# Kernel tuning notes

Hardware: AMD Instinct MI355X
Metric: run time of the kernel (lower is better)

Reference implementation:

```python
import jax, jax.numpy as jnp
import numpy as np

EPS = 1e-6
HEADS = 8


def _block_weights(gh, gw):
    # block centers at (i+0.5, j+0.5); 'cos' transform, column-normalized (sum over dim 0)
    ii, jj = np.meshgrid(np.arange(gh) + 0.5, np.arange(gw) + 0.5, indexing='ij')
    centers = np.stack([ii.ravel(), jj.ravel()], axis=-1)  # [N, 2]
    d = np.linalg.norm(centers[:, None, :] - centers[None, :, :], axis=-1)  # [N, N]
    mat = np.cos(d / d.max() * np.pi / 4.0)
    mat = mat / mat.sum(axis=0, keepdims=True)
    return jnp.asarray(mat, dtype=jnp.float32)


def setup_inputs() -> dict:
    key = jax.random.key(0)
    ks = jax.random.split(key, 5)
    B, N, W, C = 8, 256, 49, 512
    s = 1.0 / np.sqrt(C)
    return {
        'x': jax.random.normal(ks[0], (B, N, W, C), jnp.float32),
        'ln_g': jnp.ones((C,), jnp.float32),
        'ln_b': jnp.zeros((C,), jnp.float32),
        'w_qkv': jax.random.normal(ks[1], (3 * C, C), jnp.float32) * s,  # Linear(dim, 3*dim, bias=False)
        'lepe_w': jax.random.normal(ks[2], (C, 1, 5, 5), jnp.float32) * 0.2,  # depthwise 5x5
        'lepe_b': jnp.zeros((C,), jnp.float32),
        'w_out': jax.random.normal(ks[3], (C, C), jnp.float32) * s,
        'b_out': jnp.zeros((C,), jnp.float32),
    }


def reference(x, ln_g, ln_b, w_qkv, lepe_w, lepe_b, w_out, b_out):
    B, N, Wn, C = x.shape
    H = HEADS
    D = C // H
    gh = gw = int(round(N ** 0.5))   # grid of window blocks
    wh = ww = int(round(Wn ** 0.5))  # tokens per window side

    # LayerNorm over channel dim (torch eps=1e-5, biased var)
    mu = x.mean(-1, keepdims=True)
    var = x.var(-1, keepdims=True)
    xn = (x - mu) / jnp.sqrt(var + 1e-5) * ln_g + ln_b

    # qkv projection
    qkv = jnp.einsum('bnwc,oc->bnwo', xn, w_qkv)
    q, k, v = jnp.split(qkv, 3, axis=-1)  # each [B, N, W, C]

    # LePE: fold v to image [B, C, gh*wh, gw*ww], depthwise conv 5x5 pad 2, unfold back
    img = v.reshape(B, gh, gw, wh, ww, C).transpose(0, 5, 1, 3, 2, 4).reshape(B, C, gh * wh, gw * ww)
    lepe = jax.lax.conv_general_dilated(
        img, lepe_w, window_strides=(1, 1), padding=((2, 2), (2, 2)),
        dimension_numbers=('NCHW', 'OIHW', 'NCHW'), feature_group_count=C)
    lepe = lepe + lepe_b[None, :, None, None]
    lepe = lepe.reshape(B, C, gh, wh, gw, ww).transpose(0, 2, 4, 3, 5, 1).reshape(B, N, Wn, C)

    # ReLU + eps feature maps (qk_norm=False -> identity norms)
    q = jax.nn.relu(q) + EPS
    k = jax.nn.relu(k) + EPS

    # split heads: [B, H, N, W, D]
    def split_heads(t):
        return t.reshape(B, N, Wn, H, D).transpose(0, 3, 1, 2, 4)
    q, k, v = split_heads(q), split_heads(k), split_heads(v)

    # per-block k^T v state: [B, H, N, D, D]
    kv = jnp.einsum('bhnwd,bhnwe->bhnde', k, v)
    weight = _block_weights(gh, gw)  # [N, N]
    kv = jnp.einsum('ij,bhjde->bhide', weight, kv)

    k_sum = k.sum(axis=-2)  # [B, H, N, D]
    qk_sum = jnp.einsum('bhnwd,bhnd->bhnw', q, k_sum)[..., None]  # [B, H, N, W, 1]
    normalizer = jnp.einsum('ij,bhjwo->bhiwo', weight, qk_sum) + EPS

    out = jnp.einsum('bhnwd,bhnde->bhnwe', q, kv) / normalizer  # [B, H, N, W, D]
    out = out.transpose(0, 2, 3, 1, 4).reshape(B, N, Wn, C)
    out = out + lepe
    return jnp.einsum('bnwc,oc->bnwo', out, w_out) + b_out
```

## Files before the change

kernel.cpp:

```cpp
#include <hip/hip_runtime.h>
#include <cstdint>

typedef unsigned short u16;
typedef unsigned int   u32;
typedef u16   u16x8 __attribute__((ext_vector_type(8)));
typedef float f32x4 __attribute__((ext_vector_type(4)));
typedef __bf16 bf16x8 __attribute__((ext_vector_type(8)));

#define NB    256
#define WTOK  49
#define CH    512
#define HEADS 8
#define DH    64
#define TOK   100352
#define CO    1536

__device__ __forceinline__ u16 f2bf(float f) {
  u32 u = __float_as_uint(f);
  u = (u + 0x7FFFu + ((u >> 16) & 1u)) >> 16;
  return (u16)u;
}
__device__ __forceinline__ float bf2f(u16 u) { return __uint_as_float(((u32)u) << 16); }

__device__ __forceinline__ void load_lds16(const void* g, void* l) {
  __builtin_amdgcn_global_load_lds(
      reinterpret_cast<__attribute__((address_space(1))) void*>(reinterpret_cast<uintptr_t>(g)),
      reinterpret_cast<__attribute__((address_space(3))) void*>(reinterpret_cast<uintptr_t>(l)),
      16, 0, 0);
}

__global__ void cvt_f32_bf16(const float* __restrict__ in, u16* __restrict__ out, int n8) {
  int i = blockIdx.x * 256 + threadIdx.x;
  if (i < n8) {
    f32x4 a = *(const f32x4*)(in + (long)i * 8);
    f32x4 b = *(const f32x4*)(in + (long)i * 8 + 4);
    u16x8 o;
    o[0]=f2bf(a[0]); o[1]=f2bf(a[1]); o[2]=f2bf(a[2]); o[3]=f2bf(a[3]);
    o[4]=f2bf(b[0]); o[5]=f2bf(b[1]); o[6]=f2bf(b[2]); o[7]=f2bf(b[3]);
    *(u16x8*)(out + (long)i * 8) = o;
  }
}

__global__ void prep_wle(const float* __restrict__ lepe_w, float* __restrict__ wle) {
  int i = blockIdx.x * 256 + threadIdx.x;
  if (i < 12800) {
    int c = i / 25, kk = i % 25;
    wle[kk * 512 + c] = lepe_w[i];
  }
}

__global__ void weight_kernel(u16* __restrict__ Wbf, float* __restrict__ Wt) {
  int j = blockIdx.x, i = threadIdx.x;
  float iy = (float)(i >> 4) + 0.5f, ix = (float)(i & 15) + 0.5f;
  float jy = (float)(j >> 4) + 0.5f, jx = (float)(j & 15) + 0.5f;
  float dy = iy - jy, dx = ix - jx;
  float d = sqrtf(dy * dy + dx * dx);
  const float dmax = 21.213203435596427f;
  float m = cosf(d * (0.78539816339744831f / dmax));
  __shared__ float red[256];
  red[i] = m;
  __syncthreads();
  for (int s = 128; s > 0; s >>= 1) {
    if (i < s) red[i] += red[i + s];
    __syncthreads();
  }
  float w = m / red[0];
  Wbf[i * 256 + j] = f2bf(w);
  Wt[j * 256 + i] = w;
}

__global__ __launch_bounds__(256) void ln_kernel(const float* __restrict__ x,
                                                 const float* __restrict__ g,
                                                 const float* __restrict__ bta,
                                                 u16* __restrict__ xn) {
  int wave = threadIdx.x >> 6, lane = threadIdx.x & 63;
  long t = (long)blockIdx.x * 4 + wave;
  const float* xp = x + t * CH + lane * 8;
  f32x4 a = *(const f32x4*)xp;
  f32x4 b = *(const f32x4*)(xp + 4);
  float s  = a[0]+a[1]+a[2]+a[3]+b[0]+b[1]+b[2]+b[3];
  float sq = a[0]*a[0]+a[1]*a[1]+a[2]*a[2]+a[3]*a[3]+b[0]*b[0]+b[1]*b[1]+b[2]*b[2]+b[3]*b[3];
  for (int m = 1; m < 64; m <<= 1) { s += __shfl_xor(s, m); sq += __shfl_xor(sq, m); }
  float mu = s * (1.0f / 512.0f);
  float var = sq * (1.0f / 512.0f) - mu * mu;
  float rstd = rsqrtf(var + 1e-5f);
  const float* gp = g + lane * 8;
  const float* bp = bta + lane * 8;
  f32x4 g0 = *(const f32x4*)gp, g1 = *(const f32x4*)(gp + 4);
  f32x4 b0 = *(const f32x4*)bp, b1 = *(const f32x4*)(bp + 4);
  u16x8 o;
  o[0] = f2bf((a[0]-mu)*rstd*g0[0] + b0[0]);
  o[1] = f2bf((a[1]-mu)*rstd*g0[1] + b0[1]);
  o[2] = f2bf((a[2]-mu)*rstd*g0[2] + b0[2]);
  o[3] = f2bf((a[3]-mu)*rstd*g0[3] + b0[3]);
  o[4] = f2bf((b[0]-mu)*rstd*g1[0] + b1[0]);
  o[5] = f2bf((b[1]-mu)*rstd*g1[1] + b1[1]);
  o[6] = f2bf((b[2]-mu)*rstd*g1[2] + b1[2]);
  o[7] = f2bf((b[3]-mu)*rstd*g1[3] + b1[3]);
  *(u16x8*)(xn + t * CH + lane * 8) = o;
}

template <int KT>
__device__ __forceinline__ void kstep8(char* sm, const u16* sA, const u16* sB,
                                       int t, int lane_off, int wm, int wn,
                                       f32x4 (&acc)[8][4]) {
  const char* base = sm + (KT & 3) * 32768 + lane_off;
  char* wbp = sm + ((KT + 3) & 3) * 32768 + t * 16;
  if constexpr (KT + 3 < 16) {
    load_lds16(sA + (KT + 3) * 32, wbp);
    load_lds16(sA + (KT + 3) * 32 + 65536, wbp + 8192);
  }
  bf16x8 bfr[4], afr[4];
#pragma unroll
  for (int n = 0; n < 4; n++) bfr[n] = *(const bf16x8*)(base + 16384 + wn * 4096 + n * 1024);
#pragma unroll
  for (int m = 0; m < 4; m++) afr[m] = *(const bf16x8*)(base + wm * 8192 + m * 1024);
  __builtin_amdgcn_s_barrier();
  __builtin_amdgcn_s_setprio(1);
#pragma unroll
  for (int m = 0; m < 4; m++)
#pragma unroll
    for (int n = 0; n < 4; n++)
      acc[m][n] = __builtin_amdgcn_mfma_f32_16x16x32_bf16(afr[m], bfr[n], acc[m][n], 0, 0, 0);
  __builtin_amdgcn_s_setprio(0);
  __builtin_amdgcn_s_barrier();
  if constexpr (KT + 3 < 16) {
    load_lds16(sB + (KT + 3) * 32, wbp + 16384);
    load_lds16(sB + (KT + 3) * 32 + 65536, wbp + 24576);
  }
#pragma unroll
  for (int m = 0; m < 4; m++) afr[m] = *(const bf16x8*)(base + wm * 8192 + (4 + m) * 1024);
  __builtin_amdgcn_s_barrier();
  __builtin_amdgcn_s_setprio(1);
#pragma unroll
  for (int m = 0; m < 4; m++)
#pragma unroll
    for (int n = 0; n < 4; n++)
      acc[4 + m][n] = __builtin_amdgcn_mfma_f32_16x16x32_bf16(afr[m], bfr[n], acc[4 + m][n], 0, 0, 0);
  __builtin_amdgcn_s_setprio(0);
  if constexpr (KT < 13) {
    asm volatile("s_waitcnt vmcnt(8)" ::: "memory");
  } else if constexpr (KT == 13) {
    asm volatile("s_waitcnt vmcnt(4)" ::: "memory");
  } else if constexpr (KT == 14) {
    asm volatile("s_waitcnt vmcnt(0)" ::: "memory");
  }
  if constexpr (KT < 15) __builtin_amdgcn_s_barrier();
}

template <int EPI>
__global__ __launch_bounds__(512, 2)
void gemm8(const u16* __restrict__ A, const u16* __restrict__ B,
           void* __restrict__ C, const float* __restrict__ bias, int N, int nbn) {
  __shared__ __align__(16) char sm[131072];
  const int nwg = gridDim.x;
  const int bid = blockIdx.x;
  const int cpx = nwg >> 3;
  const int vid = (bid & 7) * cpx + (bid >> 3);
  const int bn = vid % nbn, bm = vid / nbn;
  const int t = threadIdx.x;
  const int lane = t & 63, wave = t >> 6;
  const int wm = wave >> 2, wn = wave & 3;
  const int fr = lane & 15, fq = lane >> 4;
  const int lane_off = (fr >> 1) * 128 + ((((fr & 1) << 2) + fq) ^ (fr >> 1)) * 16;
  const int sl = (t & 7) ^ ((t >> 3) & 7);
  const u16* sA = A + ((long)bm * 256 + ((t >> 3) << 1) + (sl >> 2)) * 512 + (sl & 3) * 8;
  const u16* sB = B + ((long)bn * 256 + ((t >> 3) << 1) + (sl >> 2)) * 512 + (sl & 3) * 8;
  f32x4 acc[8][4] = {};
#pragma unroll
  for (int kt = 0; kt < 3; kt++) {
    char* d = sm + kt * 32768 + t * 16;
    load_lds16(sA + kt * 32, d);
    load_lds16(sA + kt * 32 + 65536, d + 8192);
    load_lds16(sB + kt * 32, d + 16384);
    load_lds16(sB + kt * 32 + 65536, d + 24576);
  }
  asm volatile("s_waitcnt vmcnt(8)" ::: "memory");
  __builtin_amdgcn_s_barrier();
  kstep8<0>(sm, sA, sB, t, lane_off, wm, wn, acc);
  kstep8<1>(sm, sA, sB, t, lane_off, wm, wn, acc);
  kstep8<2>(sm, sA, sB, t, lane_off, wm, wn, acc);
  kstep8<3>(sm, sA, sB, t, lane_off, wm, wn, acc);
  kstep8<4>(sm, sA, sB, t, lane_off, wm, wn, acc);
  kstep8<5>(sm, sA, sB, t, lane_off, wm, wn, acc);
  kstep8<6>(sm, sA, sB, t, lane_off, wm, wn, acc);
  kstep8<7>(sm, sA, sB, t, lane_off, wm, wn, acc);
  kstep8<8>(sm, sA, sB, t, lane_off, wm, wn, acc);
  kstep8<9>(sm, sA, sB, t, lane_off, wm, wn, acc);
  kstep8<10>(sm, sA, sB, t, lane_off, wm, wn, acc);
  kstep8<11>(sm, sA, sB, t, lane_off, wm, wn, acc);
  kstep8<12>(sm, sA, sB, t, lane_off, wm, wn, acc);
  kstep8<13>(sm, sA, sB, t, lane_off, wm, wn, acc);
  kstep8<14>(sm, sA, sB, t, lane_off, wm, wn, acc);
  kstep8<15>(sm, sA, sB, t, lane_off, wm, wn, acc);
  const long r0 = (long)bm * 256 + wm * 128 + fq * 4;
  const int c0 = bn * 256 + wn * 64 + fr;
#pragma unroll
  for (int m = 0; m < 8; m++) {
#pragma unroll
    for (int n = 0; n < 4; n++) {
      int c = c0 + n * 16;
#pragma unroll
      for (int jj = 0; jj < 4; jj++) {
        long r = r0 + m * 16 + jj;
        float v = acc[m][n][jj];
        if (EPI == 1) {
          if (c < 1024) v = fmaxf(v, 0.0f) + 1e-6f;
          ((u16*)C)[r * N + c] = f2bf(v);
        } else if (EPI == 2) {
          ((float*)C)[r * N + c] = v + bias[c];
        } else {
          ((u16*)C)[r * N + c] = f2bf(v);
        }
      }
    }
  }
}

template <int EPI>
__global__ __launch_bounds__(256)
void gemm_bt(const u16* __restrict__ A, const u16* __restrict__ B,
             void* __restrict__ C, const float* __restrict__ bias,
             int M, int N, int K, long sAb, long sBb, long sCb) {
  __shared__ u16 As[128 * 32];
  __shared__ u16 Bs[128 * 32];
  const int tid = threadIdx.x;
  const int lane = tid & 63;
  const int wave = tid >> 6;
  const int fr = lane & 15, fq = lane >> 4;
  const int wr = (wave >> 1) * 64, wc = (wave & 1) * 64;
  const long bm = blockIdx.y, bn = blockIdx.x, bz = blockIdx.z;
  const u16* Ab = A + bz * sAb + bm * 128 * (long)K;
  const u16* Bb = B + bz * sBb + bn * 128 * (long)K;
  const int srow = tid >> 2;
  const int scol = (tid & 3) * 8;
  f32x4 acc[4][4] = {};
  for (int k0 = 0; k0 < K; k0 += 32) {
    load_lds16(Ab + (long)srow * K + k0 + scol, As + tid * 8);
    load_lds16(Ab + (long)(srow + 64) * K + k0 + scol, As + 2048 + tid * 8);
    load_lds16(Bb + (long)srow * K + k0 + scol, Bs + tid * 8);
    load_lds16(Bb + (long)(srow + 64) * K + k0 + scol, Bs + 2048 + tid * 8);
    __syncthreads();
    bf16x8 af[4], bf[4];
#pragma unroll
    for (int m = 0; m < 4; m++) af[m] = *(const bf16x8*)&As[(wr + m * 16 + fr) * 32 + fq * 8];
#pragma unroll
    for (int n = 0; n < 4; n++) bf[n] = *(const bf16x8*)&Bs[(wc + n * 16 + fr) * 32 + fq * 8];
#pragma unroll
    for (int m = 0; m < 4; m++)
#pragma unroll
      for (int n = 0; n < 4; n++)
        acc[m][n] = __builtin_amdgcn_mfma_f32_16x16x32_bf16(af[m], bf[n], acc[m][n], 0, 0, 0);
    __syncthreads();
  }
#pragma unroll
  for (int m = 0; m < 4; m++) {
    int r0 = wr + m * 16 + fq * 4;
#pragma unroll
    for (int n = 0; n < 4; n++) {
      int c = (int)bn * 128 + wc + n * 16 + fr;
#pragma unroll
      for (int jj = 0; jj < 4; jj++) {
        long r = bm * 128 + r0 + jj;
        float v = acc[m][n][jj];
        if (EPI == 1) { if (c < 1024) v = fmaxf(v, 0.0f) + 1e-6f; }
        if (EPI == 2) {
          ((float*)C)[bz * sCb + r * N + c] = v + bias[c];
        } else {
          ((u16*)C)[bz * sCb + r * N + c] = f2bf(v);
        }
      }
    }
  }
}

__global__ __launch_bounds__(256)
void fold_v(const u16* __restrict__ qkv, u16* __restrict__ vimg) {
  long i = (long)blockIdx.x * 256 + threadIdx.x;
  int tok = (int)(i >> 6);
  int c0 = ((int)i & 63) * 8;
  int w = tok % WTOK, n = tok / WTOK;
  int b = n >> 8, blk = n & 255;
  int gi = blk >> 4, gj = blk & 15;
  int wi = w / 7, wj = w - wi * 7;
  int y = gi * 7 + wi + 2, x = gj * 7 + wj + 2;
  u16x8 v = *(const u16x8*)(qkv + (long)tok * CO + 1024 + c0);
  *(u16x8*)(vimg + (((long)(b * 116 + y)) * 116 + x) * 512 + c0) = v;
}

__global__ __launch_bounds__(256)
void zero_border(u16* __restrict__ vimg) {
  int y = blockIdx.x, b = blockIdx.y;
  int tid = threadIdx.x;
  u16* row = vimg + ((long)(b * 116 + y)) * 116 * 512;
  u16x8 z = {};
  if (y < 2 || y >= 114) {
    for (int i = tid; i < 116 * 512 / 8; i += 256) *(u16x8*)(row + i * 8) = z;
  } else {
    int col = tid >> 6;
    int x = (col < 2) ? col : 112 + col;
    *(u16x8*)(row + x * 512 + (tid & 63) * 8) = z;
  }
}

__global__ __launch_bounds__(256)
void lepe_conv2(const u16* __restrict__ vimg, const float* __restrict__ wle,
                const float* __restrict__ lb, u16* __restrict__ lepe) {
  int b = blockIdx.z, y = blockIdx.y;
  int tid = threadIdx.x;
  int c0 = (tid & 63) * 8;
  int x = blockIdx.x * 4 + (tid >> 6);
  float acc[8];
  {
    f32x4 b0 = *(const f32x4*)(lb + c0);
    f32x4 b1 = *(const f32x4*)(lb + c0 + 4);
#pragma unroll
    for (int i = 0; i < 4; i++) { acc[i] = b0[i]; acc[4 + i] = b1[i]; }
  }
  const u16* base = vimg + (((long)(b * 116 + y)) * 116 + x) * 512 + c0;
#pragma unroll
  for (int ky = 0; ky < 5; ky++) {
#pragma unroll
    for (int kx = 0; kx < 5; kx++) {
      u16x8 v8 = *(const u16x8*)(base + ((long)ky * 116 + kx) * 512);
      const float* wp = wle + (ky * 5 + kx) * 512 + c0;
      f32x4 w0 = *(const f32x4*)wp, w1 = *(const f32x4*)(wp + 4);
#pragma unroll
      for (int i = 0; i < 4; i++) {
        acc[i] += bf2f(v8[i]) * w0[i];
        acc[4 + i] += bf2f(v8[4 + i]) * w1[i];
      }
    }
  }
  int gi = y / 7, wi = y - gi * 7;
  int gj = x / 7, wj = x - gj * 7;
  long tok0 = ((long)(b * NB + gi * 16 + gj)) * WTOK + wi * 7 + wj;
  u16x8 o;
#pragma unroll
  for (int i = 0; i < 8; i++) o[i] = f2bf(acc[i]);
  *(u16x8*)(lepe + tok0 * CH + c0) = o;
}

__global__ __launch_bounds__(256)
void kv_local_kernel(const u16* __restrict__ qkv, u16* __restrict__ KVl,
                     float* __restrict__ qk_sum) {
  int n = blockIdx.x, h = blockIdx.y, b = blockIdx.z;
  int bh = b * HEADS + h;
  long tbase = ((long)(b * NB + n)) * WTOK;
  __shared__ u16 kT[64 * 72];
  __shared__ u16 vT[64 * 72];
  __shared__ u16 qs[49 * 72];
  __shared__ float ksum[64];
  __shared__ float qkp[256];
  int tid = threadIdx.x;
  for (int i = tid; i < (64 * 72) / 2; i += 256) {
    ((u32*)kT)[i] = 0;
    ((u32*)vT)[i] = 0;
  }
  __syncthreads();
  {
    int w = tid >> 3, d0 = (tid & 7) * 8;
    u16x8 k8 = *(const u16x8*)(qkv + (tbase + w) * CO + 512 + h * 64 + d0);
    u16x8 v8 = *(const u16x8*)(qkv + (tbase + w) * CO + 1024 + h * 64 + d0);
#pragma unroll
    for (int i = 0; i < 8; i++) { kT[(d0 + i) * 72 + w] = k8[i]; vT[(d0 + i) * 72 + w] = v8[i]; }
    int w2 = w + 32;
    if (w2 < WTOK) {
      u16x8 k82 = *(const u16x8*)(qkv + (tbase + w2) * CO + 512 + h * 64 + d0);
      u16x8 v82 = *(const u16x8*)(qkv + (tbase + w2) * CO + 1024 + h * 64 + d0);
#pragma unroll
      for (int i = 0; i < 8; i++) { kT[(d0 + i) * 72 + w2] = k82[i]; vT[(d0 + i) * 72 + w2] = v82[i]; }
    }
    if (tid < 196) {
      int wq = tid >> 2, dq = (tid & 3) * 16;
      u16x8 q0 = *(const u16x8*)(qkv + (tbase + wq) * CO + h * 64 + dq);
      u16x8 q1 = *(const u16x8*)(qkv + (tbase + wq) * CO + h * 64 + dq + 8);
      *(u16x8*)&qs[wq * 72 + dq] = q0;
      *(u16x8*)&qs[wq * 72 + dq + 8] = q1;
    }
  }
  __syncthreads();
  if (tid < 64) {
    float s = 0.0f;
#pragma unroll
    for (int c = 0; c < 9; c++) {
      u16x8 r = *(const u16x8*)&kT[tid * 72 + c * 8];
#pragma unroll
      for (int i = 0; i < 8; i++) s += bf2f(r[i]);
    }
    ksum[tid] = s;
  }
  __syncthreads();
  if (tid < 196) {
    int w = tid >> 2, d0 = (tid & 3) * 16;
    float s = 0.0f;
#pragma unroll
    for (int i = 0; i < 16; i++) s += bf2f(qs[w * 72 + d0 + i]) * ksum[d0 + i];
    qkp[tid] = s;
  }
  __syncthreads();
  if (tid < WTOK) {
    float s = qkp[tid * 4] + qkp[tid * 4 + 1] + qkp[tid * 4 + 2] + qkp[tid * 4 + 3];
    qk_sum[((long)bh * NB + n) * WTOK + tid] = s;
  }
  int lane = tid & 63, wave = tid >> 6;
  int fr = lane & 15, fq = lane >> 4;
  f32x4 acc[4] = {};
#pragma unroll
  for (int ks = 0; ks < 2; ks++) {
    bf16x8 a = *(const bf16x8*)&kT[(wave * 16 + fr) * 72 + ks * 32 + fq * 8];
#pragma unroll
    for (int n4 = 0; n4 < 4; n4++) {
      bf16x8 bb = *(const bf16x8*)&vT[(n4 * 16 + fr) * 72 + ks * 32 + fq * 8];
      acc[n4] = __builtin_amdgcn_mfma_f32_16x16x32_bf16(a, bb, acc[n4], 0, 0, 0);
    }
  }
  long obase = ((long)bh * NB + n) * 4096;
#pragma unroll
  for (int n4 = 0; n4 < 4; n4++)
#pragma unroll
    for (int jj = 0; jj < 4; jj++) {
      int d = wave * 16 + fq * 4 + jj;
      int e = n4 * 16 + fr;
      KVl[obase + d * 64 + e] = f2bf(acc[n4][jj]);
    }
}

__global__ __launch_bounds__(256)
void transpose_kv(const u16* __restrict__ in, u16* __restrict__ out) {
  int dt = blockIdx.x, jt = blockIdx.y, bh = blockIdx.z;
  __shared__ u16 t[64 * 72];
  int tid = threadIdx.x;
  {
    int jr = tid >> 2, c0 = (tid & 3) * 16;
    const u16* ip = in + ((long)bh * NB + jt * 64 + jr) * 4096 + dt * 64 + c0;
    *(u16x8*)&t[jr * 72 + c0] = *(const u16x8*)ip;
    *(u16x8*)&t[jr * 72 + c0 + 8] = *(const u16x8*)(ip + 8);
  }
  __syncthreads();
  {
    int der = tid >> 2, j0 = (tid & 3) * 16;
    u16x8 o0, o1;
#pragma unroll
    for (int i = 0; i < 8; i++) o0[i] = t[(j0 + i) * 72 + der];
#pragma unroll
    for (int i = 0; i < 8; i++) o1[i] = t[(j0 + 8 + i) * 72 + der];
    u16* op = out + ((long)bh * 4096 + dt * 64 + der) * 256 + jt * 64 + j0;
    *(u16x8*)op = o0;
    *(u16x8*)(op + 8) = o1;
  }
}

__global__ __launch_bounds__(256)
void norm_kernel(const float* __restrict__ Wt, const float* __restrict__ qk_sum,
                 float* __restrict__ inv_norm) {
  int bh = blockIdx.x, tid = threadIdx.x;
  __shared__ float qk[NB * WTOK];
  for (int i = tid; i < NB * WTOK; i += 256) qk[i] = qk_sum[(long)bh * NB * WTOK + i];
  __syncthreads();
  float acc[WTOK];
#pragma unroll
  for (int w = 0; w < WTOK; w++) acc[w] = 0.0f;
  for (int j = 0; j < NB; j++) {
    float wv = Wt[j * NB + tid];
#pragma unroll
    for (int w = 0; w < WTOK; w++) acc[w] += wv * qk[j * WTOK + w];
  }
  long ob = ((long)bh * NB + tid) * WTOK;
#pragma unroll
  for (int w = 0; w < WTOK; w++) inv_norm[ob + w] = 1.0f / (acc[w] + 1e-6f);
}

__global__ __launch_bounds__(256)
void attn_out_kernel(const u16* __restrict__ qkv, const u16* __restrict__ kvm,
                     const float* __restrict__ inv_norm, const u16* __restrict__ lepe,
                     u16* __restrict__ ebuf) {
  int n = blockIdx.x, h = blockIdx.y, b = blockIdx.z;
  int bh = b * HEADS + h;
  long tbase = ((long)(b * NB + n)) * WTOK;
  __shared__ u16 qs[64 * 72];
  __shared__ u16 kvT[64 * 72];
  __shared__ float inv[WTOK];
  int tid = threadIdx.x;
  if (tid < 196) {
    int w = tid >> 2, d0 = (tid & 3) * 16;
    u16x8 q0 = *(const u16x8*)(qkv + (tbase + w) * CO + h * 64 + d0);
    u16x8 q1 = *(const u16x8*)(qkv + (tbase + w) * CO + h * 64 + d0 + 8);
    *(u16x8*)&qs[w * 72 + d0] = q0;
    *(u16x8*)&qs[w * 72 + d0 + 8] = q1;
  }
  {
    int d = tid >> 2, e0 = (tid & 3) * 16;
    const u16* kp = kvm + ((long)bh * NB + n) * 4096 + d * 64 + e0;
    u16x8 k0 = *(const u16x8*)kp;
    u16x8 k1 = *(const u16x8*)(kp + 8);
#pragma unroll
    for (int i = 0; i < 8; i++) { kvT[(e0 + i) * 72 + d] = k0[i]; kvT[(e0 + 8 + i) * 72 + d] = k1[i]; }
  }
  if (tid < WTOK) inv[tid] = inv_norm[((long)bh * NB + n) * WTOK + tid];
  __syncthreads();
  int lane = tid & 63, wave = tid >> 6;
  int fr = lane & 15, fq = lane >> 4;
  f32x4 acc[4] = {};
#pragma unroll
  for (int ks = 0; ks < 2; ks++) {
    bf16x8 a = *(const bf16x8*)&qs[(wave * 16 + fr) * 72 + ks * 32 + fq * 8];
#pragma unroll
    for (int n4 = 0; n4 < 4; n4++) {
      bf16x8 bb = *(const bf16x8*)&kvT[(n4 * 16 + fr) * 72 + ks * 32 + fq * 8];
      acc[n4] = __builtin_amdgcn_mfma_f32_16x16x32_bf16(a, bb, acc[n4], 0, 0, 0);
    }
  }
#pragma unroll
  for (int n4 = 0; n4 < 4; n4++)
#pragma unroll
    for (int jj = 0; jj < 4; jj++) {
      int w = wave * 16 + fq * 4 + jj;
      if (w < WTOK) {
        int e = n4 * 16 + fr;
        long off = (tbase + w) * CH + h * 64 + e;
        float v = acc[n4][jj] * inv[w] + bf2f(lepe[off]);
        ebuf[off] = f2bf(v);
      }
    }
}

static const size_t OFF_XN    = 0;
static const size_t OFF_QKV   = 102760448;
static const size_t OFF_KVL   = OFF_QKV + 308281344;
static const size_t OFF_KVT   = OFF_KVL + 134217728;
static const size_t OFF_QKS   = OFF_KVT + 134217728;
static const size_t OFF_INV   = OFF_QKS + 3211264;
static const size_t OFF_WBF   = OFF_INV + 3211264;
static const size_t OFF_WTF   = OFF_WBF + 131072;
static const size_t OFF_WQKVB = OFF_WTF + 262144;
static const size_t OFF_WOUTB = OFF_WQKVB + 1572864;
static const size_t OFF_WLE   = OFF_WOUTB + 524288;

extern "C" void kernel_launch(void* const* d_in, const int* in_sizes, int n_in,
                              void* d_out, int out_size, void* d_ws, size_t ws_size,
                              hipStream_t stream) {
  const float* x      = (const float*)d_in[0];
  const float* ln_g   = (const float*)d_in[1];
  const float* ln_b   = (const float*)d_in[2];
  const float* w_qkv  = (const float*)d_in[3];
  const float* lepe_w = (const float*)d_in[4];
  const float* lepe_b = (const float*)d_in[5];
  const float* w_out  = (const float*)d_in[6];
  const float* b_out  = (const float*)d_in[7];
  float* out = (float*)d_out;
  char* ws = (char*)d_ws;

  u16*   xn     = (u16*)(ws + OFF_XN);
  u16*   lepe   = (u16*)(ws + OFF_XN);
  u16*   qkv    = (u16*)(ws + OFF_QKV);
  u16*   KVl    = (u16*)(ws + OFF_KVL);
  u16*   kvm    = (u16*)(ws + OFF_KVL);
  u16*   vimg   = (u16*)(ws + OFF_KVT);
  u16*   KVT    = (u16*)(ws + OFF_KVT);
  u16*   ebuf   = (u16*)(ws + OFF_KVT);
  float* qks    = (float*)(ws + OFF_QKS);
  float* invn   = (float*)(ws + OFF_INV);
  u16*   Wbf    = (u16*)(ws + OFF_WBF);
  float* Wt     = (float*)(ws + OFF_WTF);
  u16*   wqkvb  = (u16*)(ws + OFF_WQKVB);
  u16*   woutb  = (u16*)(ws + OFF_WOUTB);
  float* wle    = (float*)(ws + OFF_WLE);

  cvt_f32_bf16<<<384, 256, 0, stream>>>(w_qkv, wqkvb, 98304);
  cvt_f32_bf16<<<128, 256, 0, stream>>>(w_out, woutb, 32768);
  prep_wle<<<50, 256, 0, stream>>>(lepe_w, wle);
  weight_kernel<<<256, 256, 0, stream>>>(Wbf, Wt);
  zero_border<<<dim3(116, 8), 256, 0, stream>>>(vimg);

  ln_kernel<<<25088, 256, 0, stream>>>(x, ln_g, ln_b, xn);

  gemm8<1><<<2352, 512, 0, stream>>>(xn, wqkvb, (void*)qkv, nullptr, CO, 6);

  fold_v<<<25088, 256, 0, stream>>>(qkv, vimg);
  lepe_conv2<<<dim3(28, 112, 8), 256, 0, stream>>>(vimg, wle, lepe_b, lepe);

  kv_local_kernel<<<dim3(NB, HEADS, 8), 256, 0, stream>>>(qkv, KVl, qks);

  transpose_kv<<<dim3(64, 4, 64), 256, 0, stream>>>(KVl, KVT);

  gemm_bt<0><<<dim3(32, 2, 64), 256, 0, stream>>>(Wbf, KVT, (void*)kvm, nullptr,
                                                  NB, 4096, NB,
                                                  0, (long)4096 * 256, (long)256 * 4096);

  norm_kernel<<<64, 256, 0, stream>>>(Wt, qks, invn);

  attn_out_kernel<<<dim3(NB, HEADS, 8), 256, 0, stream>>>(qkv, kvm, invn, lepe, ebuf);

  gemm8<2><<<784, 512, 0, stream>>>(ebuf, woutb, (void*)out, b_out, CH, 2);
}
```

Measured before the change: 1.086 ms.

## Rewrite LePE depthwise conv with register sliding window over rows

The depthwise 5x5 conv kernel now has each thread produce 14 consecutive output rows for 4 channels. It keeps a rolling 5x5 window of input rows in registers, so each new row needs only 5 loads instead of 25, and the weights are held in registers for the whole thread. The goal is to cut redundant global/L2 reads of the padded image and repeated weight loads. In exchange the kernel uses more registers (launch bounds set to 2 blocks), and the grid has fewer blocks, so less parallelism is available.

After: 898.8 us. 1.21x faster.

```diff
diff --git a/kernel.cpp b/kernel.cpp
--- a/kernel.cpp
+++ b/kernel.cpp
@@ -4,6 +4,7 @@
 typedef unsigned short u16;
 typedef unsigned int   u32;
 typedef u16   u16x8 __attribute__((ext_vector_type(8)));
+typedef u16   u16x4 __attribute__((ext_vector_type(4)));
 typedef float f32x4 __attribute__((ext_vector_type(4)));
 typedef __bf16 bf16x8 __attribute__((ext_vector_type(8)));
 
@@ -303,42 +304,50 @@
   }
 }
 
-__global__ __launch_bounds__(256)
-void lepe_conv2(const u16* __restrict__ vimg, const float* __restrict__ wle,
+__global__ __launch_bounds__(256, 2)
+void lepe_conv3(const u16* __restrict__ vimg, const float* __restrict__ wle,
                 const float* __restrict__ lb, u16* __restrict__ lepe) {
-  int b = blockIdx.z, y = blockIdx.y;
-  int tid = threadIdx.x;
-  int c0 = (tid & 63) * 8;
-  int x = blockIdx.x * 4 + (tid >> 6);
-  float acc[8];
-  {
-    f32x4 b0 = *(const f32x4*)(lb + c0);
-    f32x4 b1 = *(const f32x4*)(lb + c0 + 4);
-#pragma unroll
-    for (int i = 0; i < 4; i++) { acc[i] = b0[i]; acc[4 + i] = b1[i]; }
-  }
-  const u16* base = vimg + (((long)(b * 116 + y)) * 116 + x) * 512 + c0;
-#pragma unroll
-  for (int ky = 0; ky < 5; ky++) {
-#pragma unroll
-    for (int kx = 0; kx < 5; kx++) {
-      u16x8 v8 = *(const u16x8*)(base + ((long)ky * 116 + kx) * 512);
-      const float* wp = wle + (ky * 5 + kx) * 512 + c0;
-      f32x4 w0 = *(const f32x4*)wp, w1 = *(const f32x4*)(wp + 4);
-#pragma unroll
-      for (int i = 0; i < 4; i++) {
-        acc[i] += bf2f(v8[i]) * w0[i];
-        acc[4 + i] += bf2f(v8[4 + i]) * w1[i];
+  const int tid = threadIdx.x;
+  const int c0 = (tid & 127) * 4;
+  const int x  = blockIdx.x * 2 + (tid >> 7);
+  const int ys = blockIdx.y * 14;
+  const int b  = blockIdx.z;
+  f32x4 wv[25];
+#pragma unroll
+  for (int k = 0; k < 25; k++) wv[k] = *(const f32x4*)(wle + k * 512 + c0);
+  const f32x4 bias = *(const f32x4*)(lb + c0);
+  const u16* rbase = vimg + (((long)(b * 116 + ys)) * 116 + x) * 512 + c0;
+  u16x4 win[5][5];
+#pragma unroll
+  for (int j = 0; j < 4; j++) {
+    const u16* rp = rbase + (long)j * (116 * 512);
+#pragma unroll
+    for (int kx = 0; kx < 5; kx++) win[j][kx] = *(const u16x4*)(rp + kx * 512);
+  }
+  const int gj = x / 7, wj = x - gj * 7;
+  u16* ob = lepe + (((long)(b * 256 + blockIdx.y * 32 + gj)) * 49 + wj) * 512 + c0;
+#pragma unroll
+  for (int i = 0; i < 14; i++) {
+    {
+      const u16* rp = rbase + (long)(i + 4) * (116 * 512);
+#pragma unroll
+      for (int kx = 0; kx < 5; kx++) win[(i + 4) % 5][kx] = *(const u16x4*)(rp + kx * 512);
+    }
+    f32x4 acc = bias;
+#pragma unroll
+    for (int s = 0; s < 5; s++)
+#pragma unroll
+      for (int kx = 0; kx < 5; kx++) {
+        u16x4 v = win[(i + s) % 5][kx];
+        f32x4 w = wv[s * 5 + kx];
+#pragma unroll
+        for (int c = 0; c < 4; c++) acc[c] += bf2f(v[c]) * w[c];
       }
-    }
-  }
-  int gi = y / 7, wi = y - gi * 7;
-  int gj = x / 7, wj = x - gj * 7;
-  long tok0 = ((long)(b * NB + gi * 16 + gj)) * WTOK + wi * 7 + wj;
-  u16x8 o;
-#pragma unroll
-  for (int i = 0; i < 8; i++) o[i] = f2bf(acc[i]);
-  *(u16x8*)(lepe + tok0 * CH + c0) = o;
+    u16x4 o;
+#pragma unroll
+    for (int c = 0; c < 4; c++) o[c] = f2bf(acc[c]);
+    *(u16x4*)(ob + ((i / 7) * 784 + (i % 7) * 7) * 512) = o;
+  }
 }
 
 __global__ __launch_bounds__(256)
@@ -578,7 +587,7 @@
   gemm8<1><<<2352, 512, 0, stream>>>(xn, wqkvb, (void*)qkv, nullptr, CO, 6);
 
   fold_v<<<25088, 256, 0, stream>>>(qkv, vimg);
-  lepe_conv2<<<dim3(28, 112, 8), 256, 0, stream>>>(vimg, wle, lepe_b, lepe);
+  lepe_conv3<<<dim3(56, 8, 8), 256, 0, stream>>>(vimg, wle, lepe_b, lepe);
 
   kv_local_kernel<<<dim3(NB, HEADS, 8), 256, 0, stream>>>(qkv, KVl, qks);
 
```
